# Optimization experiments

Hardware: AMD Instinct MI355X
Metric: run time of the kernel (lower is better)

Reference implementation:

```python
import jax, jax.numpy as jnp
import numpy as np

D_MODEL = 1024; D_STATE = 64; D_CONV = 4; EXPAND = 2; HEADDIM = 128; NGROUPS = 1; CHUNK = 256
D_INNER = EXPAND * D_MODEL            # 2048
NHEADS = D_INNER // HEADDIM           # 16
CONV_DIM = D_INNER + 2 * NGROUPS * D_STATE   # 2176
D_IN_PROJ = 2 * D_INNER + 2 * NGROUPS * D_STATE + NHEADS  # 4240
B = 4; G = 256; L = 2048
EPS = 1e-5


def setup_inputs() -> dict:
    key = jax.random.key(0)
    ks = jax.random.split(key, 12)
    def nrm(k, shape, s=0.02):
        return jax.random.normal(k, shape, jnp.float32) * s
    return dict(
        local_repr=jax.random.normal(ks[0], (B, L, D_MODEL), jnp.float32),
        global_repr=jax.random.normal(ks[1], (B, G, D_MODEL), jnp.float32),
        norm1_w=jnp.ones((D_MODEL,), jnp.float32), norm1_b=jnp.zeros((D_MODEL,), jnp.float32),
        norm2_w=jnp.ones((D_MODEL,), jnp.float32), norm2_b=jnp.zeros((D_MODEL,), jnp.float32),
        norm3_w=jnp.ones((D_MODEL,), jnp.float32), norm3_b=jnp.zeros((D_MODEL,), jnp.float32),
        in_proj_w=nrm(ks[2], (D_IN_PROJ, D_MODEL)),
        conv_w=nrm(ks[3], (CONV_DIM, D_CONV), 0.2),
        conv_b=jnp.zeros((CONV_DIM,), jnp.float32),
        dt_bias=jnp.log(jnp.expm1(jax.random.uniform(ks[4], (NHEADS,), jnp.float32, 1e-3, 0.1))),
        A_log=jnp.log(jax.random.uniform(ks[5], (NHEADS,), jnp.float32, 1.0, 16.0)),
        D_skip=jnp.ones((NHEADS,), jnp.float32),
        ssd_norm_w=jnp.ones((D_INNER,), jnp.float32),
        out_proj_w=nrm(ks[6], (D_MODEL, D_INNER)),
        ffn_w1=nrm(ks[7], (D_MODEL // 2, D_MODEL)),
        ffn_b1=jnp.zeros((D_MODEL // 2,), jnp.float32),
        ffn_w2=nrm(ks[8], (D_MODEL, D_MODEL // 2)),
        ffn_b2=jnp.zeros((D_MODEL,), jnp.float32),
    )


def _ln(x, w, b):
    mu = jnp.mean(x, axis=-1, keepdims=True)
    var = jnp.mean((x - mu) ** 2, axis=-1, keepdims=True)
    return (x - mu) * jax.lax.rsqrt(var + EPS) * w + b


def _segsum(a):
    # a: (..., T) -> (..., T, T) lower-triangular sums a[j+1..i]
    T = a.shape[-1]
    cs = jnp.cumsum(a, axis=-1)
    diff = cs[..., :, None] - cs[..., None, :]
    mask = jnp.tril(jnp.ones((T, T), bool))
    return jnp.where(mask, diff, -jnp.inf)


def _ssd(xdt, a_dt, Bh, Ch):
    # xdt: (b,t,h,p) = x*dt ; a_dt: (b,t,h) = dt*A ; Bh,Ch: (b,t,h,n)
    b, t, h, p = xdt.shape
    n = Bh.shape[-1]
    c = t // CHUNK
    X = xdt.reshape(b, c, CHUNK, h, p)
    Bc = Bh.reshape(b, c, CHUNK, h, n)
    Cc = Ch.reshape(b, c, CHUNK, h, n)
    Ac = a_dt.reshape(b, c, CHUNK, h).transpose(0, 3, 1, 2)  # (b,h,c,k)
    A_cum = jnp.cumsum(Ac, axis=-1)
    Lm = jnp.exp(_segsum(Ac))                                # (b,h,c,k,k)
    Y_diag = jnp.einsum('bckhn,bcshn,bhcks,bcshp->bckhp', Cc, Bc, Lm, X)
    decay_states = jnp.exp(A_cum[..., -1:] - A_cum)          # (b,h,c,k)
    states = jnp.einsum('bckhn,bhck,bckhp->bchpn', Bc, decay_states, X)
    A_last = jnp.pad(A_cum[..., -1], ((0, 0), (0, 0), (1, 0)))
    decay_chunk = jnp.exp(_segsum(A_last))                   # (b,h,c+1,c+1)
    states = jnp.concatenate([jnp.zeros_like(states[:, :1]), states], axis=1)
    new_states = jnp.einsum('bhzc,bchpn->bzhpn', decay_chunk, states)
    states_in = new_states[:, :-1]                           # (b,c,h,p,n)
    out_decay = jnp.exp(A_cum)                               # (b,h,c,k)
    Y_off = jnp.einsum('bckhn,bchpn,bhck->bckhp', Cc, states_in, out_decay)
    return (Y_diag + Y_off).reshape(b, t, h, p)


def _mamba2(x, in_proj_w, conv_w, conv_b, dt_bias, A_log, D_skip, ssd_norm_w, out_proj_w):
    b, t, _ = x.shape
    zxbcdt = x @ in_proj_w.T                                  # (b,t,D_IN_PROJ)
    z = zxbcdt[..., :D_INNER]
    xBC = zxbcdt[..., D_INNER:D_INNER + CONV_DIM]
    dt = jax.nn.softplus(zxbcdt[..., D_INNER + CONV_DIM:] + dt_bias)  # (b,t,h)
    # causal depthwise conv1d, kernel D_CONV
    xp = jnp.pad(xBC, ((0, 0), (D_CONV - 1, 0), (0, 0)))
    xBC = sum(xp[:, i:i + t, :] * conv_w[:, i] for i in range(D_CONV)) + conv_b
    xBC = jax.nn.silu(xBC)
    xs = xBC[..., :D_INNER].reshape(b, t, NHEADS, HEADDIM)
    Bm = xBC[..., D_INNER:D_INNER + NGROUPS * D_STATE].reshape(b, t, NGROUPS, D_STATE)
    Cm = xBC[..., D_INNER + NGROUPS * D_STATE:].reshape(b, t, NGROUPS, D_STATE)
    rep = NHEADS // NGROUPS
    Bh = jnp.repeat(Bm, rep, axis=2)
    Ch = jnp.repeat(Cm, rep, axis=2)
    A = -jnp.exp(A_log)                                       # (h,)
    Y = _ssd(xs * dt[..., None], dt * A, Bh, Ch)
    y = Y + D_skip[None, None, :, None] * xs
    y = y.reshape(b, t, D_INNER)
    # gated RMSNorm (norm_before_gate=False)
    y = y * jax.nn.silu(z)
    y = y * jax.lax.rsqrt(jnp.mean(y * y, axis=-1, keepdims=True) + EPS) * ssd_norm_w
    return y @ out_proj_w.T


def reference(local_repr, global_repr, norm1_w, norm1_b, norm2_w, norm2_b, norm3_w, norm3_b,
              in_proj_w, conv_w, conv_b, dt_bias, A_log, D_skip, ssd_norm_w, out_proj_w,
              ffn_w1, ffn_b1, ffn_w2, ffn_b2):
    local_n = _ln(local_repr, norm1_w, norm1_b)
    global_n = _ln(global_repr, norm2_w, norm2_b)
    x = jnp.concatenate([global_n, local_n], axis=1)          # (B, G+L, D)
    x = _mamba2(x, in_proj_w, conv_w, conv_b, dt_bias, A_log, D_skip, ssd_norm_w, out_proj_w)
    x = x[:, -local_n.shape[1]:, :] + local_n
    x = _ln(x, norm3_w, norm3_b)
    h = jax.nn.gelu(x @ ffn_w1.T + ffn_b1, approximate=False)
    return (h @ ffn_w2.T + ffn_b2) + x
```

## Files before the change

### kernel.cpp

```cpp
#include <hip/hip_runtime.h>
#include <math.h>

#define B_ 4
#define L_ 2048
#define G_ 256
#define T_ 2304
#define DM 1024
#define DINNER 2048
#define NH 16
#define HD 128
#define NSTATE 64
#define CONVD 2176
#define DPROJ 4240
#define NPROJ_PAD 4352
#define NCHUNK 9
#define CK 256
#define EPSV 1e-5f
#define CROWS 16

typedef unsigned short bf16t;
using bf16x8 = __attribute__((ext_vector_type(8))) short;
using f32x4  = __attribute__((ext_vector_type(4))) float;

__device__ __forceinline__ float bf2f(bf16t u) {
  return __uint_as_float(((unsigned int)u) << 16);
}
__device__ __forceinline__ bf16t f2bf(float f) {
  unsigned int u = __float_as_uint(f);
  u += 0x7FFFu + ((u >> 16) & 1u);
  return (bf16t)(u >> 16);
}

__device__ __forceinline__ void g2lds16(const bf16t* g, short* l) {
  __builtin_amdgcn_global_load_lds(
      (const __attribute__((address_space(1))) unsigned int*)g,
      (__attribute__((address_space(3))) unsigned int*)l, 16, 0, 0);
}

__device__ __forceinline__ int2 xcd_swz(int tiles_n) {
  int gx = gridDim.x, gy = gridDim.y;
  int id = blockIdx.y * gx + blockIdx.x;
  int cpx = (gx * gy) >> 3;
  int L = (id & 7) * cpx + (id >> 3);
  return make_int2(L % tiles_n, L / tiles_n);
}

__device__ __forceinline__ float2 block_reduce2(float a, float b) {
  __shared__ float sa[4], sb[4];
  #pragma unroll
  for (int off = 32; off > 0; off >>= 1) {
    a += __shfl_down(a, off, 64);
    b += __shfl_down(b, off, 64);
  }
  int lane = threadIdx.x & 63, wid = threadIdx.x >> 6;
  if (lane == 0) { sa[wid] = a; sb[wid] = b; }
  __syncthreads();
  return make_float2(sa[0] + sa[1] + sa[2] + sa[3], sb[0] + sb[1] + sb[2] + sb[3]);
}

__global__ __launch_bounds__(256) void ln_cvt_kernel(
    const float* __restrict__ localr, const float* __restrict__ globalr,
    const float* __restrict__ w1, const float* __restrict__ b1,
    const float* __restrict__ w2, const float* __restrict__ b2,
    bf16t* __restrict__ x, const float* __restrict__ inpw,
    bf16t* __restrict__ inpw_bf) {
  int blk = blockIdx.x;
  if (blk < B_ * T_) {
    int t = blk % T_, b = blk / T_;
    const float *src, *w, *bb;
    if (t < G_) { src = globalr + ((long)b * G_ + t) * DM;        w = w2; bb = b2; }
    else        { src = localr  + ((long)b * L_ + (t - G_)) * DM; w = w1; bb = b1; }
    int d = threadIdx.x * 4;
    float4 v = *(const float4*)&src[d];
    float s = v.x + v.y + v.z + v.w;
    float sq = v.x * v.x + v.y * v.y + v.z * v.z + v.w * v.w;
    float2 r2 = block_reduce2(s, sq);
    float mu = r2.x * (1.f / DM);
    float var = r2.y * (1.f / DM) - mu * mu;
    float rstd = rsqrtf(var + EPSV);
    float4 wv = *(const float4*)&w[d];
    float4 bv = *(const float4*)&bb[d];
    ushort4 o;
    o.x = f2bf((v.x - mu) * rstd * wv.x + bv.x);
    o.y = f2bf((v.y - mu) * rstd * wv.y + bv.y);
    o.z = f2bf((v.z - mu) * rstd * wv.z + bv.z);
    o.w = f2bf((v.w - mu) * rstd * wv.w + bv.w);
    *(ushort4*)&x[(long)blk * DM + d] = o;
  } else {
    long i = (long)(blk - B_ * T_) * 1024 + threadIdx.x * 4;
    const long nreal = (long)DPROJ * DM, ntot = (long)NPROJ_PAD * DM;
    if (i < ntot) {
      ushort4 o = {0, 0, 0, 0};
      if (i < nreal) {
        float4 v = *(const float4*)&inpw[i];
        o.x = f2bf(v.x); o.y = f2bf(v.y); o.z = f2bf(v.z); o.w = f2bf(v.w);
      }
      *(ushort4*)&inpw_bf[i] = o;
    }
  }
}

template<int EPI, bool OFFS, int K>
__global__ __launch_bounds__(512, 2) void gemm_wide(
    const bf16t* __restrict__ A, const bf16t* __restrict__ W,
    bf16t* __restrict__ Cb, bf16t* __restrict__ z, bf16t* __restrict__ xpre,
    float* __restrict__ dtr, const float* __restrict__ bias,
    const bf16t* __restrict__ res, float* __restrict__ Cf, int N) {
  __shared__ short LDS8[65536];
  int tid = threadIdx.x;
  int lane = tid & 63, w = tid >> 6;
  int wm = w >> 1, wn = w & 1;
  int l15 = lane & 15;
  int2 sz = xcd_swz(gridDim.x);
  int bn = sz.x * 128, bm = sz.y * 256;
  if (EPI == 0 && bn < DINNER && (bm % 2304) == 0) return;
  long bmA = OFFS ? ((long)(bm >> 11) * T_ + G_ + (bm & 2047)) : (long)bm;

  int csub = ((lane & 7) ^ (lane >> 3)) * 8;
  const bf16t* srcA = A + (bmA + w * 16 + (lane >> 3)) * (long)K + csub;
  const bf16t* srcW = W + (long)(bn + w * 16 + (lane >> 3)) * K + csub;
  int stageDst = w * 1024 + lane * 8;

  int off0 = l15 * 64 + (((lane >> 4) + 0) ^ (lane & 7)) * 8;
  int off1 = l15 * 64 + (((lane >> 4) + 4) ^ (lane & 7)) * 8;

  f32x4 acc[4][4] = {};
  bf16x8 af[2][2], bq[4][2];

#define STAGE2(gsrc, ldsoff) do { \
    g2lds16((gsrc), LDS8 + (ldsoff) + stageDst); \
    g2lds16((gsrc) + 8 * (long)K, LDS8 + (ldsoff) + stageDst + 512); } while (0)

  STAGE2(srcA, 0);
  STAGE2(srcA + 128 * (long)K, 8192);
  STAGE2(srcW, 49152);
  STAGE2(srcA + 64, 16384);
  STAGE2(srcA + 128 * (long)K + 64, 16384 + 8192);
  STAGE2(srcW + 64, 49152 + 8192);
  asm volatile("s_waitcnt vmcnt(6)" ::: "memory");
  __builtin_amdgcn_s_barrier();

  const int nt = K >> 6;
  for (int t = 0; t < nt; ++t) {
    int slotA = (t % 3) * 16384;
    int slotA2 = ((t + 2) % 3) * 16384;
    const short* aB = LDS8 + slotA + wm * 4096;
    const short* bB = LDS8 + 49152 + (t & 1) * 8192 + wn * 4096;

    #pragma unroll
    for (int mi = 0; mi < 2; mi++) {
      af[mi][0] = *(const bf16x8*)&aB[mi * 1024 + off0];
      af[mi][1] = *(const bf16x8*)&aB[mi * 1024 + off1];
    }
    #pragma unroll
    for (int ni = 0; ni < 2; ni++) {
      bq[ni][0] = *(const bf16x8*)&bB[ni * 1024 + off0];
      bq[ni][1] = *(const bf16x8*)&bB[ni * 1024 + off1];
    }
    if (t + 2 < nt) STAGE2(srcA + (t + 2) * 64, slotA2);
    __builtin_amdgcn_s_barrier();
    __builtin_amdgcn_s_setprio(1);
    #pragma unroll
    for (int ks = 0; ks < 2; ks++)
      #pragma unroll
      for (int mi = 0; mi < 2; mi++)
        #pragma unroll
        for (int ni = 0; ni < 2; ni++)
          acc[mi][ni] = __builtin_amdgcn_mfma_f32_16x16x32_bf16(af[mi][ks], bq[ni][ks], acc[mi][ni], 0, 0, 0);
    __builtin_amdgcn_s_setprio(0);
    __builtin_amdgcn_s_barrier();

    #pragma unroll
    for (int ni = 2; ni < 4; ni++) {
      bq[ni][0] = *(const bf16x8*)&bB[ni * 1024 + off0];
      bq[ni][1] = *(const bf16x8*)&bB[ni * 1024 + off1];
    }
    if (t + 2 < nt) STAGE2(srcA + 128 * (long)K + (t + 2) * 64, slotA2 + 8192);
    __builtin_amdgcn_s_barrier();
    __builtin_amdgcn_s_setprio(1);
    #pragma unroll
    for (int ks = 0; ks < 2; ks++)
      #pragma unroll
      for (int mi = 0; mi < 2; mi++)
        #pragma unroll
        for (int ni = 2; ni < 4; ni++)
          acc[mi][ni] = __builtin_amdgcn_mfma_f32_16x16x32_bf16(af[mi][ks], bq[ni][ks], acc[mi][ni], 0, 0, 0);
    __builtin_amdgcn_s_setprio(0);
    __builtin_amdgcn_s_barrier();

    #pragma unroll
    for (int mi = 0; mi < 2; mi++) {
      af[mi][0] = *(const bf16x8*)&aB[(mi + 2) * 1024 + off0];
      af[mi][1] = *(const bf16x8*)&aB[(mi + 2) * 1024 + off1];
    }
    if (t + 2 < nt) STAGE2(srcW + (t + 2) * 64, 49152 + (t & 1) * 8192);
    __builtin_amdgcn_s_barrier();
    __builtin_amdgcn_s_setprio(1);
    #pragma unroll
    for (int ks = 0; ks < 2; ks++)
      #pragma unroll
      for (int mi = 0; mi < 2; mi++)
        #pragma unroll
        for (int ni = 0; ni < 4; ni++)
          acc[mi + 2][ni] = __builtin_amdgcn_mfma_f32_16x16x32_bf16(af[mi][ks], bq[ni][ks], acc[mi + 2][ni], 0, 0, 0);
    __builtin_amdgcn_s_setprio(0);
    if (t + 2 < nt)      asm volatile("s_waitcnt vmcnt(6)" ::: "memory");
    else if (t + 1 < nt) asm volatile("s_waitcnt vmcnt(0)" ::: "memory");
    __builtin_amdgcn_s_barrier();
  }
#undef STAGE2

  if (EPI == 0 && bn == 4224) {
    if (wn == 0) {
      #pragma unroll
      for (int mi = 0; mi < 4; mi++)
        #pragma unroll
        for (int r = 0; r < 4; r++) {
          int row = bm + wm * 64 + mi * 16 + (lane >> 4) * 4 + r;
          dtr[(long)row * NH + l15] = acc[mi][0][r];
        }
    }
    return;
  }

  if (EPI == 2) {
    float* Cs32 = (float*)LDS8;
    #pragma unroll
    for (int pass = 0; pass < 2; pass++) {
      __syncthreads();
      if ((wm >> 1) == pass) {
        #pragma unroll
        for (int mi = 0; mi < 4; mi++)
          #pragma unroll
          for (int ni = 0; ni < 4; ni++)
            #pragma unroll
            for (int r = 0; r < 4; r++)
              Cs32[((wm & 1) * 64 + mi * 16 + (lane >> 4) * 4 + r) * 136 + wn * 64 + ni * 16 + l15] =
                  acc[mi][ni][r];
      }
      __syncthreads();
      #pragma unroll
      for (int q = 0; q < 4; q++) {
        int idx = q * 512 + tid;
        int row = idx >> 4, cg = (idx & 15) * 8;
        long grow = bm + pass * 128 + row; int gcol = bn + cg;
        float4 v0 = *(float4*)&Cs32[row * 136 + cg];
        float4 v1 = *(float4*)&Cs32[row * 136 + cg + 4];
        float4 b0 = *(const float4*)&bias[gcol];
        float4 b1 = *(const float4*)&bias[gcol + 4];
        bf16x8 rv = *(const bf16x8*)&res[grow * (long)N + gcol];
        v0.x += b0.x + bf2f((bf16t)rv[0]); v0.y += b0.y + bf2f((bf16t)rv[1]);
        v0.z += b0.z + bf2f((bf16t)rv[2]); v0.w += b0.w + bf2f((bf16t)rv[3]);
        v1.x += b1.x + bf2f((bf16t)rv[4]); v1.y += b1.y + bf2f((bf16t)rv[5]);
        v1.z += b1.z + bf2f((bf16t)rv[6]); v1.w += b1.w + bf2f((bf16t)rv[7]);
        *(float4*)&Cf[grow * (long)N + gcol] = v0;
        *(float4*)&Cf[grow * (long)N + gcol + 4] = v1;
      }
    }
    return;
  }

  bf16t* Cs = (bf16t*)LDS8;
  #pragma unroll
  for (int pass = 0; pass < 2; pass++) {
    __syncthreads();
    if ((wm >> 1) == pass) {
      #pragma unroll
      for (int mi = 0; mi < 4; mi++)
        #pragma unroll
        for (int ni = 0; ni < 4; ni++)
          #pragma unroll
          for (int r = 0; r < 4; r++)
            Cs[((wm & 1) * 64 + mi * 16 + (lane >> 4) * 4 + r) * 136 + wn * 64 + ni * 16 + l15] =
                f2bf(acc[mi][ni][r]);
    }
    __syncthreads();
    #pragma unroll
    for (int q = 0; q < 4; q++) {
      int idx = q * 512 + tid;
      int row = idx >> 4, cg = idx & 15;
      int gcol = bn + cg * 8;
      long grow = bm + pass * 128 + row;
      bf16x8 v = *(bf16x8*)&Cs[row * 136 + cg * 8];
      if (EPI == 0) {
        if (gcol < DINNER) *(bf16x8*)&z[grow * DINNER + gcol] = v;
        else               *(bf16x8*)&xpre[grow * CONVD + (gcol - DINNER)] = v;
      } else {
        *(bf16x8*)&Cb[grow * (long)N + gcol] = v;
      }
    }
  }
}

template<int EPI>
__global__ __launch_bounds__(256) void gemm_mfma(
    const bf16t* __restrict__ A, const bf16t* __restrict__ W,
    const float* __restrict__ bias, const bf16t* __restrict__ res,
    float* __restrict__ Cf, bf16t* __restrict__ Cb,
    int N, int K) {
  __shared__ __align__(16) short LDS[128 * 136];
  short* As = LDS;
  short* Ws = LDS + 128 * 32;
  int tid = threadIdx.x;
  int lane = tid & 63, w = tid >> 6;
  int wr = w >> 1, wc = w & 1;
  int2 sz = xcd_swz(gridDim.x);
  int bn = sz.x * 128, bm = sz.y * 128;

  int r1 = tid >> 2,         s1 = (((tid & 3) ^ ((r1 >> 1) & 3))) * 8;
  int r2 = (tid + 256) >> 2, s2 = (((tid & 3) ^ ((r2 >> 1) & 3))) * 8;
  const bf16t* gA1 = A + (long)(bm + r1) * K + s1;
  const bf16t* gA2 = A + (long)(bm + r2) * K + s2;
  const bf16t* gW1 = W + (long)(bn + r1) * K + s1;
  const bf16t* gW2 = W + (long)(bn + r2) * K + s2;
  short* lA1 = As + tid * 8;
  short* lA2 = As + (tid + 256) * 8;
  short* lW1 = Ws + tid * 8;
  short* lW2 = Ws + (tid + 256) * 8;

  int arow = wr * 64 + (lane & 15);
  int brow = wc * 64 + (lane & 15);
  int koff = (((lane >> 4) ^ (((lane & 15) >> 1) & 3))) * 8;

  f32x4 acc[4][4] = {};
  for (int k0 = 0; k0 < K; k0 += 32) {
    g2lds16(gA1 + k0, lA1);
    g2lds16(gA2 + k0, lA2);
    g2lds16(gW1 + k0, lW1);
    g2lds16(gW2 + k0, lW2);
    __syncthreads();
    bf16x8 af[4], bf[4];
    #pragma unroll
    for (int mi = 0; mi < 4; mi++) af[mi] = *(bf16x8*)&As[(arow + mi * 16) * 32 + koff];
    #pragma unroll
    for (int ni = 0; ni < 4; ni++) bf[ni] = *(bf16x8*)&Ws[(brow + ni * 16) * 32 + koff];
    #pragma unroll
    for (int mi = 0; mi < 4; mi++)
      #pragma unroll
      for (int ni = 0; ni < 4; ni++)
        acc[mi][ni] = __builtin_amdgcn_mfma_f32_16x16x32_bf16(af[mi], bf[ni], acc[mi][ni], 0, 0, 0);
    __syncthreads();
  }

  int rb = wr * 64 + (lane >> 4) * 4;
  int cb = wc * 64 + (lane & 15);

  __syncthreads();
  bf16t* Cs = (bf16t*)LDS;
  #pragma unroll
  for (int mi = 0; mi < 4; mi++)
    #pragma unroll
    for (int ni = 0; ni < 4; ni++)
      #pragma unroll
      for (int r = 0; r < 4; r++) {
        float v = acc[mi][ni][r];
        if (EPI == 2) {
          v += bias[bn + cb + ni * 16];
          v = 0.5f * v * (1.f + erff(v * 0.70710678118f));
        }
        Cs[(rb + mi * 16 + r) * 136 + cb + ni * 16] = f2bf(v);
      }
  __syncthreads();
  #pragma unroll
  for (int pass = 0; pass < 8; pass++) {
    int row = pass * 16 + (tid >> 4);
    int col = (tid & 15) * 8;
    bf16x8 vv = *(bf16x8*)&Cs[row * 136 + col];
    long grow = bm + row; int gcol = bn + col;
    *(bf16x8*)&Cb[grow * N + gcol] = vv;
  }
}

__global__ __launch_bounds__(256) void cumsum_kernel(
    const float* __restrict__ dtraw, const float* __restrict__ dt_bias,
    const float* __restrict__ A_log, float* __restrict__ dt,
    float* __restrict__ Acum) {
  int bid = blockIdx.x;
  int c = bid % NCHUNK; int hh = bid / NCHUNK;
  int h = hh % NH; int b = hh / NH;
  int k = threadIdx.x;
  float a = -__expf(A_log[h]);
  long t = (long)b * T_ + c * CK + k;
  float v0 = dtraw[t * NH + h] + dt_bias[h];
  float dtv = (v0 > 20.f) ? v0 : log1pf(__expf(v0));
  dt[t * NH + h] = dtv;
  float v = dtv * a;
  __shared__ float buf[2][CK];
  int cur = 0;
  buf[0][k] = v; __syncthreads();
  for (int off = 1; off < CK; off <<= 1) {
    float tv = buf[cur][k];
    if (k >= off) tv += buf[cur][k - off];
    buf[1 - cur][k] = tv; cur ^= 1; __syncthreads();
  }
  Acum[(long)bid * CK + k] = buf[cur][k];
}

__global__ __launch_bounds__(256) void conv_kernel(
    const bf16t* __restrict__ xpre, const float* __restrict__ cw,
    const float* __restrict__ cb, bf16t* __restrict__ out) {
  int gt = blockIdx.x * 256 + threadIdx.x;
  int cg = gt % 272; int rt = gt / 272;
  int c0 = cg * 8;
  long r0 = (long)rt * CROWS;
  int t0 = (int)(r0 % T_);

  float wreg[4][8];
  #pragma unroll
  for (int j = 0; j < 8; j++) {
    float4 wa = *(const float4*)&cw[(c0 + j) * 4];
    wreg[0][j] = wa.x; wreg[1][j] = wa.y; wreg[2][j] = wa.z; wreg[3][j] = wa.w;
  }
  float4 cb0 = *(const float4*)&cb[c0];
  float4 cb1 = *(const float4*)&cb[c0 + 4];
  float bias[8] = {cb0.x, cb0.y, cb0.z, cb0.w, cb1.x, cb1.y, cb1.z, cb1.w};

  bf16x8 win[4];
  #pragma unroll
  for (int i = 0; i < 3; i++) {
    if (t0 - 3 + i >= 0) win[i] = *(const bf16x8*)&xpre[(r0 - 3 + i) * CONVD + c0];
    else                 win[i] = bf16x8{0,0,0,0,0,0,0,0};
  }

  #pragma unroll
  for (int k = 0; k < CROWS; k++) {
    win[3] = *(const bf16x8*)&xpre[(r0 + k) * CONVD + c0];
    float acc[8];
    #pragma unroll
    for (int j = 0; j < 8; j++) acc[j] = bias[j];
    #pragma unroll
    for (int i = 0; i < 4; i++)
      #pragma unroll
      for (int j = 0; j < 8; j++)
        acc[j] += bf2f((bf16t)win[i][j]) * wreg[i][j];
    bf16x8 o;
    #pragma unroll
    for (int j = 0; j < 8; j++) {
      float s = acc[j] / (1.f + __expf(-acc[j]));
      o[j] = (short)f2bf(s);
    }
    *(bf16x8*)&out[(r0 + k) * CONVD + c0] = o;
    win[0] = win[1]; win[1] = win[2]; win[2] = win[3];
  }
}

__global__ __launch_bounds__(256) void chunk_states_kernel(
    const bf16t* __restrict__ xbc, const float* __restrict__ dt,
    const float* __restrict__ Acum, float* __restrict__ cs) {
  int bid = blockIdx.x;
  int h = bid & 15; int bc = bid >> 4;
  int c = bc & 7; int b = bc >> 3;
  int tid = threadIdx.x;
  int lane = tid & 63, w = tid >> 6;
  long tch = (long)b * T_ + c * CK;
  int acb = ((b * NH + h) * NCHUNK + c) * CK;
  float Alast = Acum[acb + CK - 1];

  __shared__ bf16t Xt[128][72];
  __shared__ bf16t Bt[64][72];
  __shared__ float wk[64];

  f32x4 acc[8] = {};
  for (int kb = 0; kb < 4; kb++) {
    int s0 = kb * 64;
    __syncthreads();
    if (tid < 64)
      wk[tid] = __expf(Alast - Acum[acb + s0 + tid]) * dt[(tch + s0 + tid) * NH + h];
    __syncthreads();
    for (int e = tid; e < 64 * 32; e += 256) {
      int s = e & 63, p4 = e >> 6;
      ushort4 u = *(const ushort4*)&xbc[(tch + s0 + s) * CONVD + h * HD + p4 * 4];
      float wv = wk[s];
      Xt[p4 * 4 + 0][s] = f2bf(bf2f(u.x) * wv);
      Xt[p4 * 4 + 1][s] = f2bf(bf2f(u.y) * wv);
      Xt[p4 * 4 + 2][s] = f2bf(bf2f(u.z) * wv);
      Xt[p4 * 4 + 3][s] = f2bf(bf2f(u.w) * wv);
    }
    for (int e = tid; e < 64 * 16; e += 256) {
      int s = e & 63, n4 = e >> 6;
      ushort4 u = *(const ushort4*)&xbc[(tch + s0 + s) * CONVD + DINNER + n4 * 4];
      Bt[n4 * 4 + 0][s] = u.x; Bt[n4 * 4 + 1][s] = u.y;
      Bt[n4 * 4 + 2][s] = u.z; Bt[n4 * 4 + 3][s] = u.w;
    }
    __syncthreads();
    #pragma unroll
    for (int ks = 0; ks < 2; ks++) {
      int koff = (lane >> 4) * 8 + ks * 32;
      bf16x8 bfr = *(bf16x8*)&Bt[w * 16 + (lane & 15)][koff];
      #pragma unroll
      for (int mi = 0; mi < 8; mi++) {
        bf16x8 af = *(bf16x8*)&Xt[mi * 16 + (lane & 15)][koff];
        acc[mi] = __builtin_amdgcn_mfma_f32_16x16x32_bf16(af, bfr, acc[mi], 0, 0, 0);
      }
    }
  }
  int cbid = (b * NCHUNK + c) * NH + h;
  float* out = cs + (long)cbid * HD * NSTATE;
  int n = w * 16 + (lane & 15);
  #pragma unroll
  for (int mi = 0; mi < 8; mi++) {
    #pragma unroll
    for (int r = 0; r < 4; r++) {
      int p = mi * 16 + (lane >> 4) * 4 + r;
      out[p * NSTATE + n] = acc[mi][r];
    }
  }
}

__global__ __launch_bounds__(256) void state_pass_kernel(
    float* __restrict__ cs, const float* __restrict__ Acum) {
  int bh = blockIdx.x;
  int b = bh / NH, h = bh % NH;
  int e0 = blockIdx.y * 1024 + threadIdx.x;
  for (int q = 0; q < 4; q++) {
    int e = e0 + q * 256;
    float s = 0.f;
    for (int c = 0; c < NCHUNK; c++) {
      long idx = ((long)(b * NCHUNK + c) * NH + h) * (HD * NSTATE) + e;
      if (c < NCHUNK - 1) {
        float tmp = cs[idx];
        cs[idx] = s;
        float g = __expf(Acum[((b * NH + h) * NCHUNK + c) * CK + CK - 1]);
        s = s * g + tmp;
      } else {
        cs[idx] = s;
      }
    }
  }
}

__global__ __launch_bounds__(256) void ssd_y_kernel(
    const bf16t* __restrict__ xbc, const float* __restrict__ dt,
    const float* __restrict__ Acum, const float* __restrict__ sin_,
    const float* __restrict__ Dskip, bf16t* __restrict__ Y) {
  int bid = blockIdx.x;
  int h = bid & 15; int bc = bid >> 4;
  int c = 1 + (bc & 7); int b = bc >> 3;
  int rt = blockIdx.y;
  int tid = threadIdx.x;
  int lane = tid & 63, w = tid >> 6;
  int wr = w >> 1, wc = w & 1;
  long tch = (long)b * T_ + c * CK;
  long tbase = tch + rt * 128;
  int acb = ((b * NH + h) * NCHUNK + c) * CK;

  __shared__ bf16t Cs[128][72];
  __shared__ bf16t Bs[64][72];
  __shared__ bf16t Xt[128][72];
  __shared__ bf16t Sm[128][72];
  __shared__ float Akl[128];
  __shared__ float Asl[64];
  __shared__ float dts[64];

  for (int e = tid; e < 128 * 8; e += 256) {
    int row = e >> 3, seg = (e & 7) * 8;
    *(bf16x8*)&Cs[row][seg] =
        *(const bf16x8*)&xbc[(tbase + row) * CONVD + DINNER + NSTATE + seg];
  }
  if (tid < 128) Akl[tid] = Acum[acb + rt * 128 + tid];

  f32x4 acc[4][4] = {};
  int nsb = 2 * (rt + 1);
  for (int sb = 0; sb < nsb; sb++) {
    int s0 = sb * 64;
    __syncthreads();
    if (tid < 64) {
      Asl[tid] = Acum[acb + s0 + tid];
      dts[tid] = dt[(tch + s0 + tid) * NH + h];
    }
    __syncthreads();
    for (int e = tid; e < 64 * 8; e += 256) {
      int row = e >> 3, seg = (e & 7) * 8;
      *(bf16x8*)&Bs[row][seg] =
          *(const bf16x8*)&xbc[(tch + s0 + row) * CONVD + DINNER + seg];
    }
    for (int e = tid; e < 64 * 32; e += 256) {
      int s = e & 63, p4 = e >> 6;
      ushort4 u = *(const ushort4*)&xbc[(tch + s0 + s) * CONVD + h * HD + p4 * 4];
      float dtv = dts[s];
      Xt[p4 * 4 + 0][s] = f2bf(bf2f(u.x) * dtv);
      Xt[p4 * 4 + 1][s] = f2bf(bf2f(u.y) * dtv);
      Xt[p4 * 4 + 2][s] = f2bf(bf2f(u.z) * dtv);
      Xt[p4 * 4 + 3][s] = f2bf(bf2f(u.w) * dtv);
    }
    __syncthreads();
    {
      f32x4 sacc[2][4] = {};
      int rw0 = w * 32;
      #pragma unroll
      for (int ks = 0; ks < 2; ks++) {
        int koff = (lane >> 4) * 8 + ks * 32;
        bf16x8 a0 = *(bf16x8*)&Cs[rw0 + (lane & 15)][koff];
        bf16x8 a1 = *(bf16x8*)&Cs[rw0 + 16 + (lane & 15)][koff];
        #pragma unroll
        for (int ni = 0; ni < 4; ni++) {
          bf16x8 bfr = *(bf16x8*)&Bs[ni * 16 + (lane & 15)][koff];
          sacc[0][ni] = __builtin_amdgcn_mfma_f32_16x16x32_bf16(a0, bfr, sacc[0][ni], 0, 0, 0);
          sacc[1][ni] = __builtin_amdgcn_mfma_f32_16x16x32_bf16(a1, bfr, sacc[1][ni], 0, 0, 0);
        }
      }
      #pragma unroll
      for (int mi = 0; mi < 2; mi++) {
        #pragma unroll
        for (int ni = 0; ni < 4; ni++) {
          #pragma unroll
          for (int r = 0; r < 4; r++) {
            int row = rw0 + mi * 16 + (lane >> 4) * 4 + r;
            int scol = ni * 16 + (lane & 15);
            int kglob = rt * 128 + row;
            int sglob = s0 + scol;
            float val = 0.f;
            if (sglob <= kglob) val = sacc[mi][ni][r] * __expf(Akl[row] - Asl[scol]);
            Sm[row][scol] = f2bf(val);
          }
        }
      }
    }
    __syncthreads();
    #pragma unroll
    for (int ks = 0; ks < 2; ks++) {
      int koff = (lane >> 4) * 8 + ks * 32;
      bf16x8 af[4], bfr[4];
      #pragma unroll
      for (int mi = 0; mi < 4; mi++) af[mi] = *(bf16x8*)&Sm[wr * 64 + mi * 16 + (lane & 15)][koff];
      #pragma unroll
      for (int ni = 0; ni < 4; ni++) bfr[ni] = *(bf16x8*)&Xt[wc * 64 + ni * 16 + (lane & 15)][koff];
      #pragma unroll
      for (int mi = 0; mi < 4; mi++)
        #pragma unroll
        for (int ni = 0; ni < 4; ni++)
          acc[mi][ni] = __builtin_amdgcn_mfma_f32_16x16x32_bf16(af[mi], bfr[ni], acc[mi][ni], 0, 0, 0);
    }
  }

  float ekr[16];
  #pragma unroll
  for (int mi = 0; mi < 4; mi++)
    #pragma unroll
    for (int r = 0; r < 4; r++)
      ekr[mi * 4 + r] = __expf(Akl[wr * 64 + mi * 16 + (lane >> 4) * 4 + r]);

  int cbid = (b * NCHUNK + c) * NH + h;
  const float* sinb = sin_ + (long)cbid * HD * NSTATE;
  #pragma unroll
  for (int ni = 0; ni < 4; ni++) {
    f32x4 offacc[4] = {};
    int p = wc * 64 + ni * 16 + (lane & 15);
    #pragma unroll
    for (int ks = 0; ks < 2; ks++) {
      int koff = (lane >> 4) * 8 + ks * 32;
      const float* srow = sinb + p * NSTATE + koff;
      float4 sa = *(const float4*)srow;
      float4 sbv = *(const float4*)(srow + 4);
      bf16x8 bfr;
      bfr[0] = (short)f2bf(sa.x);  bfr[1] = (short)f2bf(sa.y);
      bfr[2] = (short)f2bf(sa.z);  bfr[3] = (short)f2bf(sa.w);
      bfr[4] = (short)f2bf(sbv.x); bfr[5] = (short)f2bf(sbv.y);
      bfr[6] = (short)f2bf(sbv.z); bfr[7] = (short)f2bf(sbv.w);
      #pragma unroll
      for (int mi = 0; mi < 4; mi++) {
        bf16x8 af = *(bf16x8*)&Cs[wr * 64 + mi * 16 + (lane & 15)][koff];
        offacc[mi] = __builtin_amdgcn_mfma_f32_16x16x32_bf16(af, bfr, offacc[mi], 0, 0, 0);
      }
    }
    #pragma unroll
    for (int mi = 0; mi < 4; mi++)
      #pragma unroll
      for (int r = 0; r < 4; r++)
        acc[mi][ni][r] += ekr[mi * 4 + r] * offacc[mi][r];
  }

  float dsk = Dskip[h];
  #pragma unroll
  for (int mi = 0; mi < 4; mi++) {
    #pragma unroll
    for (int r = 0; r < 4; r++) {
      int row = wr * 64 + mi * 16 + (lane >> 4) * 4 + r;
      long t = tbase + row;
      #pragma unroll
      for (int ni = 0; ni < 4; ni++) {
        int p = wc * 64 + ni * 16 + (lane & 15);
        float xsv = bf2f(xbc[t * CONVD + h * HD + p]);
        Y[t * DINNER + h * HD + p] = f2bf(acc[mi][ni][r] + dsk * xsv);
      }
    }
  }
}

__global__ __launch_bounds__(256) void gate_rms_cvt_kernel(
    const bf16t* __restrict__ z, const float* __restrict__ nw,
    bf16t* __restrict__ Y,
    const float* __restrict__ outw, const float* __restrict__ f1w,
    const float* __restrict__ f2w, bf16t* __restrict__ o_out,
    bf16t* __restrict__ o_f1, bf16t* __restrict__ o_f2) {
  int blk = blockIdx.x;
  if (blk < B_ * L_) {
    long r = (long)(blk >> 11) * T_ + G_ + (blk & 2047);
    const bf16t* zrow = z + r * DINNER;
    bf16t* yrow = Y + r * DINNER;
    int tid = threadIdx.x;
    float v[8]; float sq = 0.f;
    #pragma unroll
    for (int i = 0; i < 4; i++) {
      int d = tid * 2 + 512 * i;
      ushort2 zu = *(const ushort2*)&zrow[d];
      ushort2 yu = *(const ushort2*)&yrow[d];
      float z0 = bf2f(zu.x), z1 = bf2f(zu.y);
      float y0 = bf2f(yu.x) * (z0 / (1.f + __expf(-z0)));
      float y1 = bf2f(yu.y) * (z1 / (1.f + __expf(-z1)));
      v[2 * i] = y0; v[2 * i + 1] = y1;
      sq += y0 * y0 + y1 * y1;
    }
    float2 r2 = block_reduce2(sq, 0.f);
    float rms = rsqrtf(r2.x * (1.f / DINNER) + EPSV);
    #pragma unroll
    for (int i = 0; i < 4; i++) {
      int d = tid * 2 + 512 * i;
      ushort2 o;
      o.x = f2bf(v[2 * i] * rms * nw[d]);
      o.y = f2bf(v[2 * i + 1] * rms * nw[d + 1]);
      *(ushort2*)&yrow[d] = o;
    }
  } else {
    long i = (long)(blk - B_ * L_) * 1024 + threadIdx.x * 4;
    const long n1 = (long)DM * DINNER;
    const long n2 = (long)(DM / 2) * DM;
    const float* src; bf16t* dst; long off;
    if (i < n1) { src = outw; dst = o_out; off = i; }
    else if (i < n1 + n2) { src = f1w; dst = o_f1; off = i - n1; }
    else { src = f2w; dst = o_f2; off = i - n1 - n2; }
    float4 v = *(const float4*)&src[off];
    ushort4 o;
    o.x = f2bf(v.x); o.y = f2bf(v.y); o.z = f2bf(v.z); o.w = f2bf(v.w);
    *(ushort4*)&dst[off] = o;
  }
}

__global__ __launch_bounds__(256) void res_ln3_kernel(
    const bf16t* __restrict__ mfull, const bf16t* __restrict__ x,
    const float* __restrict__ w3, const float* __restrict__ b3,
    bf16t* __restrict__ x2) {
  int rl = blockIdx.x;
  int tl = rl & 2047, b = rl >> 11;
  long rt = (long)b * T_ + G_ + tl;
  const bf16t* m = mfull + (long)rl * DM;
  const bf16t* xr = x + rt * DM;
  int tid = threadIdx.x;
  float v[4]; float s = 0.f, sq = 0.f;
  #pragma unroll
  for (int i = 0; i < 2; i++) {
    int d = tid * 2 + 512 * i;
    ushort2 mu2 = *(const ushort2*)&m[d];
    ushort2 xu2 = *(const ushort2*)&xr[d];
    float a0 = bf2f(mu2.x) + bf2f(xu2.x);
    float a1 = bf2f(mu2.y) + bf2f(xu2.y);
    v[2 * i] = a0; v[2 * i + 1] = a1;
    s += a0 + a1; sq += a0 * a0 + a1 * a1;
  }
  float2 r2 = block_reduce2(s, sq);
  float mu = r2.x * (1.f / DM);
  float var = r2.y * (1.f / DM) - mu * mu;
  float rstd = rsqrtf(var + EPSV);
  bf16t* dst = x2 + (long)rl * DM;
  #pragma unroll
  for (int i = 0; i < 2; i++) {
    int d = tid * 2 + 512 * i;
    ushort2 o;
    o.x = f2bf((v[2 * i] - mu) * rstd * w3[d] + b3[d]);
    o.y = f2bf((v[2 * i + 1] - mu) * rstd * w3[d + 1] + b3[d + 1]);
    *(ushort2*)&dst[d] = o;
  }
}

extern "C" void kernel_launch(void* const* d_in, const int* in_sizes, int n_in,
                              void* d_out, int out_size, void* d_ws, size_t ws_size,
                              hipStream_t stream) {
  const float* localr = (const float*)d_in[0];
  const float* globalr= (const float*)d_in[1];
  const float* n1w = (const float*)d_in[2];
  const float* n1b = (const float*)d_in[3];
  const float* n2w = (const float*)d_in[4];
  const float* n2b = (const float*)d_in[5];
  const float* n3w = (const float*)d_in[6];
  const float* n3b = (const float*)d_in[7];
  const float* inpw= (const float*)d_in[8];
  const float* convw=(const float*)d_in[9];
  const float* convb=(const float*)d_in[10];
  const float* dtb = (const float*)d_in[11];
  const float* alog= (const float*)d_in[12];
  const float* dskp= (const float*)d_in[13];
  const float* ssdw= (const float*)d_in[14];
  const float* outw= (const float*)d_in[15];
  const float* f1w = (const float*)d_in[16];
  const float* f1b = (const float*)d_in[17];
  const float* f2w = (const float*)d_in[18];
  const float* f2b = (const float*)d_in[19];

  char* ws = (char*)d_ws;
  bf16t* x     = (bf16t*)(ws + 0);
  bf16t* z     = (bf16t*)(ws + 18874368);
  bf16t* mfull = (bf16t*)(ws + 18874368);
  bf16t* xpre  = (bf16t*)(ws + 56623104);
  bf16t* Yb    = (bf16t*)(ws + 56623104);
  float* dtraw = (float*)(ws + 96731136);
  float* dt    = (float*)(ws + 97320960);
  float* Acum  = (float*)(ws + 97910784);
  bf16t* xbc   = (bf16t*)(ws + 98500608);
  bf16t* x2bf  = (bf16t*)(ws + 98500608);
  bf16t* hbuf  = (bf16t*)(ws + 115277824);
  bf16t* outw_bf = (bf16t*)(ws + 123666432);
  bf16t* f1w_bf  = (bf16t*)(ws + 127860736);
  bf16t* f2w_bf  = (bf16t*)(ws + 128909312);
  float* cs    = (float*)(ws + 138608640);
  bf16t* inpw_bf = (bf16t*)(ws + 138608640);

  ln_cvt_kernel<<<B_ * T_ + 4352, 256, 0, stream>>>(
      localr, globalr, n1w, n1b, n2w, n2b, x, inpw, inpw_bf);

  gemm_wide<0, false, 1024><<<dim3(NPROJ_PAD / 128, (B_ * T_) / 256), 512, 0, stream>>>(
      x, inpw_bf, nullptr, z, xpre, dtraw, nullptr, nullptr, nullptr, NPROJ_PAD);

  cumsum_kernel<<<B_ * NH * NCHUNK, 256, 0, stream>>>(dtraw, dtb, alog, dt, Acum);

  conv_kernel<<<(B_ * T_ / CROWS) * 272 / 256, 256, 0, stream>>>(xpre, convw, convb, xbc);

  chunk_states_kernel<<<B_ * (NCHUNK - 1) * NH, 256, 0, stream>>>(xbc, dt, Acum, cs);

  state_pass_kernel<<<dim3(B_ * NH, 8), 256, 0, stream>>>(cs, Acum);

  ssd_y_kernel<<<dim3(B_ * (NCHUNK - 1) * NH, 2), 256, 0, stream>>>(
      xbc, dt, Acum, cs, dskp, Yb);

  gate_rms_cvt_kernel<<<B_ * L_ + 3072, 256, 0, stream>>>(
      z, ssdw, Yb, outw, f1w, f2w, outw_bf, f1w_bf, f2w_bf);

  gemm_wide<1, true, 2048><<<dim3(DM / 128, (B_ * L_) / 256), 512, 0, stream>>>(
      Yb, outw_bf, mfull, nullptr, nullptr, nullptr, nullptr, nullptr, nullptr, DM);

  res_ln3_kernel<<<B_ * L_, 256, 0, stream>>>(mfull, x, n3w, n3b, x2bf);

  gemm_mfma<2><<<dim3((DM / 2) / 128, (B_ * L_) / 128), 256, 0, stream>>>(
      x2bf, f1w_bf, f1b, nullptr, nullptr, hbuf, DM / 2, DM);

  gemm_wide<2, false, 512><<<dim3(DM / 128, (B_ * L_) / 256), 512, 0, stream>>>(
      hbuf, f2w_bf, nullptr, nullptr, nullptr, nullptr, f2b, x2bf, (float*)d_out, DM);
}
```

Before: 472.5 us.

## Merge conv and cumsum launches, vectorize LDS transposes and row kernels

Merges the conv and dt-cumsum kernels into a single launch that branches on block index, removing one launch. In the chunk-states and ssd_y loaders, each thread now reads four consecutive time rows and writes packed ushort4 values into the transposed LDS tiles, replacing scalar 16-bit LDS stores. The ssd_y epilogue stages accumulators through shared memory so that Y and the D-skip x input move as coalesced 16-byte vectors instead of scattered scalar accesses. The gated RMSNorm and the final LayerNorm row kernels switch to wider per-thread vector loads and stores. In exchange there are extra barriers in the epilogue and slightly more global loads in flight per thread.

```diff
diff --git a/kernel.cpp b/kernel.cpp
--- a/kernel.cpp
+++ b/kernel.cpp
@@ -17,6 +17,7 @@
 #define CK 256
 #define EPSV 1e-5f
 #define CROWS 16
+#define CONVBLKS 612
 
 typedef unsigned short bf16t;
 using bf16x8 = __attribute__((ext_vector_type(8))) short;
@@ -371,76 +372,76 @@
   }
 }
 
-__global__ __launch_bounds__(256) void cumsum_kernel(
+__global__ __launch_bounds__(256) void conv_cumsum_kernel(
+    const bf16t* __restrict__ xpre, const float* __restrict__ cw,
+    const float* __restrict__ cb, bf16t* __restrict__ out,
     const float* __restrict__ dtraw, const float* __restrict__ dt_bias,
     const float* __restrict__ A_log, float* __restrict__ dt,
     float* __restrict__ Acum) {
-  int bid = blockIdx.x;
-  int c = bid % NCHUNK; int hh = bid / NCHUNK;
-  int h = hh % NH; int b = hh / NH;
-  int k = threadIdx.x;
-  float a = -__expf(A_log[h]);
-  long t = (long)b * T_ + c * CK + k;
-  float v0 = dtraw[t * NH + h] + dt_bias[h];
-  float dtv = (v0 > 20.f) ? v0 : log1pf(__expf(v0));
-  dt[t * NH + h] = dtv;
-  float v = dtv * a;
-  __shared__ float buf[2][CK];
-  int cur = 0;
-  buf[0][k] = v; __syncthreads();
-  for (int off = 1; off < CK; off <<= 1) {
-    float tv = buf[cur][k];
-    if (k >= off) tv += buf[cur][k - off];
-    buf[1 - cur][k] = tv; cur ^= 1; __syncthreads();
-  }
-  Acum[(long)bid * CK + k] = buf[cur][k];
-}
-
-__global__ __launch_bounds__(256) void conv_kernel(
-    const bf16t* __restrict__ xpre, const float* __restrict__ cw,
-    const float* __restrict__ cb, bf16t* __restrict__ out) {
-  int gt = blockIdx.x * 256 + threadIdx.x;
-  int cg = gt % 272; int rt = gt / 272;
-  int c0 = cg * 8;
-  long r0 = (long)rt * CROWS;
-  int t0 = (int)(r0 % T_);
-
-  float wreg[4][8];
-  #pragma unroll
-  for (int j = 0; j < 8; j++) {
-    float4 wa = *(const float4*)&cw[(c0 + j) * 4];
-    wreg[0][j] = wa.x; wreg[1][j] = wa.y; wreg[2][j] = wa.z; wreg[3][j] = wa.w;
-  }
-  float4 cb0 = *(const float4*)&cb[c0];
-  float4 cb1 = *(const float4*)&cb[c0 + 4];
-  float bias[8] = {cb0.x, cb0.y, cb0.z, cb0.w, cb1.x, cb1.y, cb1.z, cb1.w};
-
-  bf16x8 win[4];
-  #pragma unroll
-  for (int i = 0; i < 3; i++) {
-    if (t0 - 3 + i >= 0) win[i] = *(const bf16x8*)&xpre[(r0 - 3 + i) * CONVD + c0];
-    else                 win[i] = bf16x8{0,0,0,0,0,0,0,0};
-  }
-
-  #pragma unroll
-  for (int k = 0; k < CROWS; k++) {
-    win[3] = *(const bf16x8*)&xpre[(r0 + k) * CONVD + c0];
-    float acc[8];
-    #pragma unroll
-    for (int j = 0; j < 8; j++) acc[j] = bias[j];
-    #pragma unroll
-    for (int i = 0; i < 4; i++)
-      #pragma unroll
-      for (int j = 0; j < 8; j++)
-        acc[j] += bf2f((bf16t)win[i][j]) * wreg[i][j];
-    bf16x8 o;
+  if (blockIdx.x < CONVBLKS) {
+    int gt = blockIdx.x * 256 + threadIdx.x;
+    int cg = gt % 272; int rt = gt / 272;
+    int c0 = cg * 8;
+    long r0 = (long)rt * CROWS;
+    int t0 = (int)(r0 % T_);
+
+    float wreg[4][8];
     #pragma unroll
     for (int j = 0; j < 8; j++) {
-      float s = acc[j] / (1.f + __expf(-acc[j]));
-      o[j] = (short)f2bf(s);
-    }
-    *(bf16x8*)&out[(r0 + k) * CONVD + c0] = o;
-    win[0] = win[1]; win[1] = win[2]; win[2] = win[3];
+      float4 wa = *(const float4*)&cw[(c0 + j) * 4];
+      wreg[0][j] = wa.x; wreg[1][j] = wa.y; wreg[2][j] = wa.z; wreg[3][j] = wa.w;
+    }
+    float4 cb0 = *(const float4*)&cb[c0];
+    float4 cb1 = *(const float4*)&cb[c0 + 4];
+    float bias[8] = {cb0.x, cb0.y, cb0.z, cb0.w, cb1.x, cb1.y, cb1.z, cb1.w};
+
+    bf16x8 win[4];
+    #pragma unroll
+    for (int i = 0; i < 3; i++) {
+      if (t0 - 3 + i >= 0) win[i] = *(const bf16x8*)&xpre[(r0 - 3 + i) * CONVD + c0];
+      else                 win[i] = bf16x8{0,0,0,0,0,0,0,0};
+    }
+
+    #pragma unroll
+    for (int k = 0; k < CROWS; k++) {
+      win[3] = *(const bf16x8*)&xpre[(r0 + k) * CONVD + c0];
+      float acc[8];
+      #pragma unroll
+      for (int j = 0; j < 8; j++) acc[j] = bias[j];
+      #pragma unroll
+      for (int i = 0; i < 4; i++)
+        #pragma unroll
+        for (int j = 0; j < 8; j++)
+          acc[j] += bf2f((bf16t)win[i][j]) * wreg[i][j];
+      bf16x8 o;
+      #pragma unroll
+      for (int j = 0; j < 8; j++) {
+        float s = acc[j] / (1.f + __expf(-acc[j]));
+        o[j] = (short)f2bf(s);
+      }
+      *(bf16x8*)&out[(r0 + k) * CONVD + c0] = o;
+      win[0] = win[1]; win[1] = win[2]; win[2] = win[3];
+    }
+  } else {
+    int bid = blockIdx.x - CONVBLKS;
+    int c = bid % NCHUNK; int hh = bid / NCHUNK;
+    int h = hh % NH; int b = hh / NH;
+    int k = threadIdx.x;
+    float a = -__expf(A_log[h]);
+    long t = (long)b * T_ + c * CK + k;
+    float v0 = dtraw[t * NH + h] + dt_bias[h];
+    float dtv = (v0 > 20.f) ? v0 : log1pf(__expf(v0));
+    dt[t * NH + h] = dtv;
+    float v = dtv * a;
+    __shared__ float buf[2][CK];
+    int cur = 0;
+    buf[0][k] = v; __syncthreads();
+    for (int off = 1; off < CK; off <<= 1) {
+      float tv = buf[cur][k];
+      if (k >= off) tv += buf[cur][k - off];
+      buf[1 - cur][k] = tv; cur ^= 1; __syncthreads();
+    }
+    Acum[(long)bid * CK + k] = buf[cur][k];
   }
 }
 
@@ -467,20 +468,44 @@
     if (tid < 64)
       wk[tid] = __expf(Alast - Acum[acb + s0 + tid]) * dt[(tch + s0 + tid) * NH + h];
     __syncthreads();
-    for (int e = tid; e < 64 * 32; e += 256) {
-      int s = e & 63, p4 = e >> 6;
-      ushort4 u = *(const ushort4*)&xbc[(tch + s0 + s) * CONVD + h * HD + p4 * 4];
-      float wv = wk[s];
-      Xt[p4 * 4 + 0][s] = f2bf(bf2f(u.x) * wv);
-      Xt[p4 * 4 + 1][s] = f2bf(bf2f(u.y) * wv);
-      Xt[p4 * 4 + 2][s] = f2bf(bf2f(u.z) * wv);
-      Xt[p4 * 4 + 3][s] = f2bf(bf2f(u.w) * wv);
-    }
-    for (int e = tid; e < 64 * 16; e += 256) {
-      int s = e & 63, n4 = e >> 6;
-      ushort4 u = *(const ushort4*)&xbc[(tch + s0 + s) * CONVD + DINNER + n4 * 4];
-      Bt[n4 * 4 + 0][s] = u.x; Bt[n4 * 4 + 1][s] = u.y;
-      Bt[n4 * 4 + 2][s] = u.z; Bt[n4 * 4 + 3][s] = u.w;
+    for (int e = tid; e < 16 * 32; e += 256) {
+      int s4 = (e & 15) * 4, p4 = e >> 4;
+      const bf16t* base = &xbc[(tch + s0 + s4) * CONVD + h * HD + p4 * 4];
+      ushort4 u0 = *(const ushort4*)(base);
+      ushort4 u1 = *(const ushort4*)(base + CONVD);
+      ushort4 u2 = *(const ushort4*)(base + 2 * CONVD);
+      ushort4 u3 = *(const ushort4*)(base + 3 * CONVD);
+      float w0 = wk[s4], w1 = wk[s4 + 1], w2 = wk[s4 + 2], w3 = wk[s4 + 3];
+      ushort4 pk;
+      pk.x = f2bf(bf2f(u0.x) * w0); pk.y = f2bf(bf2f(u1.x) * w1);
+      pk.z = f2bf(bf2f(u2.x) * w2); pk.w = f2bf(bf2f(u3.x) * w3);
+      *(ushort4*)&Xt[p4 * 4 + 0][s4] = pk;
+      pk.x = f2bf(bf2f(u0.y) * w0); pk.y = f2bf(bf2f(u1.y) * w1);
+      pk.z = f2bf(bf2f(u2.y) * w2); pk.w = f2bf(bf2f(u3.y) * w3);
+      *(ushort4*)&Xt[p4 * 4 + 1][s4] = pk;
+      pk.x = f2bf(bf2f(u0.z) * w0); pk.y = f2bf(bf2f(u1.z) * w1);
+      pk.z = f2bf(bf2f(u2.z) * w2); pk.w = f2bf(bf2f(u3.z) * w3);
+      *(ushort4*)&Xt[p4 * 4 + 2][s4] = pk;
+      pk.x = f2bf(bf2f(u0.w) * w0); pk.y = f2bf(bf2f(u1.w) * w1);
+      pk.z = f2bf(bf2f(u2.w) * w2); pk.w = f2bf(bf2f(u3.w) * w3);
+      *(ushort4*)&Xt[p4 * 4 + 3][s4] = pk;
+    }
+    for (int e = tid; e < 16 * 16; e += 256) {
+      int s4 = (e & 15) * 4, n4 = e >> 4;
+      const bf16t* base = &xbc[(tch + s0 + s4) * CONVD + DINNER + n4 * 4];
+      ushort4 u0 = *(const ushort4*)(base);
+      ushort4 u1 = *(const ushort4*)(base + CONVD);
+      ushort4 u2 = *(const ushort4*)(base + 2 * CONVD);
+      ushort4 u3 = *(const ushort4*)(base + 3 * CONVD);
+      ushort4 pk;
+      pk.x = u0.x; pk.y = u1.x; pk.z = u2.x; pk.w = u3.x;
+      *(ushort4*)&Bt[n4 * 4 + 0][s4] = pk;
+      pk.x = u0.y; pk.y = u1.y; pk.z = u2.y; pk.w = u3.y;
+      *(ushort4*)&Bt[n4 * 4 + 1][s4] = pk;
+      pk.x = u0.z; pk.y = u1.z; pk.z = u2.z; pk.w = u3.z;
+      *(ushort4*)&Bt[n4 * 4 + 2][s4] = pk;
+      pk.x = u0.w; pk.y = u1.w; pk.z = u2.w; pk.w = u3.w;
+      *(ushort4*)&Bt[n4 * 4 + 3][s4] = pk;
     }
     __syncthreads();
     #pragma unroll
@@ -546,8 +571,9 @@
 
   __shared__ bf16t Cs[128][72];
   __shared__ bf16t Bs[64][72];
-  __shared__ bf16t Xt[128][72];
-  __shared__ bf16t Sm[128][72];
+  __shared__ __align__(16) bf16t XtSm[2][128][72];
+  bf16t (*Xt)[72] = XtSm[0];
+  bf16t (*Sm)[72] = XtSm[1];
   __shared__ float Akl[128];
   __shared__ float Asl[64];
   __shared__ float dts[64];
@@ -574,14 +600,27 @@
       *(bf16x8*)&Bs[row][seg] =
           *(const bf16x8*)&xbc[(tch + s0 + row) * CONVD + DINNER + seg];
     }
-    for (int e = tid; e < 64 * 32; e += 256) {
-      int s = e & 63, p4 = e >> 6;
-      ushort4 u = *(const ushort4*)&xbc[(tch + s0 + s) * CONVD + h * HD + p4 * 4];
-      float dtv = dts[s];
-      Xt[p4 * 4 + 0][s] = f2bf(bf2f(u.x) * dtv);
-      Xt[p4 * 4 + 1][s] = f2bf(bf2f(u.y) * dtv);
-      Xt[p4 * 4 + 2][s] = f2bf(bf2f(u.z) * dtv);
-      Xt[p4 * 4 + 3][s] = f2bf(bf2f(u.w) * dtv);
+    for (int e = tid; e < 16 * 32; e += 256) {
+      int s4 = (e & 15) * 4, p4 = e >> 4;
+      const bf16t* base = &xbc[(tch + s0 + s4) * CONVD + h * HD + p4 * 4];
+      ushort4 u0 = *(const ushort4*)(base);
+      ushort4 u1 = *(const ushort4*)(base + CONVD);
+      ushort4 u2 = *(const ushort4*)(base + 2 * CONVD);
+      ushort4 u3 = *(const ushort4*)(base + 3 * CONVD);
+      float d0 = dts[s4], d1 = dts[s4 + 1], d2 = dts[s4 + 2], d3 = dts[s4 + 3];
+      ushort4 pk;
+      pk.x = f2bf(bf2f(u0.x) * d0); pk.y = f2bf(bf2f(u1.x) * d1);
+      pk.z = f2bf(bf2f(u2.x) * d2); pk.w = f2bf(bf2f(u3.x) * d3);
+      *(ushort4*)&Xt[p4 * 4 + 0][s4] = pk;
+      pk.x = f2bf(bf2f(u0.y) * d0); pk.y = f2bf(bf2f(u1.y) * d1);
+      pk.z = f2bf(bf2f(u2.y) * d2); pk.w = f2bf(bf2f(u3.y) * d3);
+      *(ushort4*)&Xt[p4 * 4 + 1][s4] = pk;
+      pk.x = f2bf(bf2f(u0.z) * d0); pk.y = f2bf(bf2f(u1.z) * d1);
+      pk.z = f2bf(bf2f(u2.z) * d2); pk.w = f2bf(bf2f(u3.z) * d3);
+      *(ushort4*)&Xt[p4 * 4 + 2][s4] = pk;
+      pk.x = f2bf(bf2f(u0.w) * d0); pk.y = f2bf(bf2f(u1.w) * d1);
+      pk.z = f2bf(bf2f(u2.w) * d2); pk.w = f2bf(bf2f(u3.w) * d3);
+      *(ushort4*)&Xt[p4 * 4 + 3][s4] = pk;
     }
     __syncthreads();
     {
@@ -671,18 +710,32 @@
   }
 
   float dsk = Dskip[h];
+  float* Sf = (float*)&XtSm[0][0][0];
   #pragma unroll
-  for (int mi = 0; mi < 4; mi++) {
-    #pragma unroll
-    for (int r = 0; r < 4; r++) {
-      int row = wr * 64 + mi * 16 + (lane >> 4) * 4 + r;
-      long t = tbase + row;
-      #pragma unroll
-      for (int ni = 0; ni < 4; ni++) {
-        int p = wc * 64 + ni * 16 + (lane & 15);
-        float xsv = bf2f(xbc[t * CONVD + h * HD + p]);
-        Y[t * DINNER + h * HD + p] = f2bf(acc[mi][ni][r] + dsk * xsv);
-      }
+  for (int rh = 0; rh < 2; rh++) {
+    __syncthreads();
+    if (wr == rh) {
+      #pragma unroll
+      for (int mi = 0; mi < 4; mi++)
+        #pragma unroll
+        for (int ni = 0; ni < 4; ni++)
+          #pragma unroll
+          for (int r = 0; r < 4; r++)
+            Sf[(mi * 16 + (lane >> 4) * 4 + r) * 130 + wc * 64 + ni * 16 + (lane & 15)] =
+                acc[mi][ni][r];
+    }
+    __syncthreads();
+    #pragma unroll
+    for (int g = 0; g < 4; g++) {
+      int idx = g * 256 + tid;
+      int row = idx >> 4, cg = (idx & 15) * 8;
+      long t = tbase + rh * 64 + row;
+      bf16x8 xv = *(const bf16x8*)&xbc[t * CONVD + h * HD + cg];
+      bf16x8 o;
+      #pragma unroll
+      for (int j = 0; j < 8; j++)
+        o[j] = (short)f2bf(Sf[row * 130 + cg + j] + dsk * bf2f((bf16t)xv[j]));
+      *(bf16x8*)&Y[t * DINNER + h * HD + cg] = o;
     }
   }
 }
@@ -699,28 +752,25 @@
     const bf16t* zrow = z + r * DINNER;
     bf16t* yrow = Y + r * DINNER;
     int tid = threadIdx.x;
+    int d = tid * 8;
+    bf16x8 zu = *(const bf16x8*)&zrow[d];
+    bf16x8 yu = *(const bf16x8*)&yrow[d];
     float v[8]; float sq = 0.f;
     #pragma unroll
-    for (int i = 0; i < 4; i++) {
-      int d = tid * 2 + 512 * i;
-      ushort2 zu = *(const ushort2*)&zrow[d];
-      ushort2 yu = *(const ushort2*)&yrow[d];
-      float z0 = bf2f(zu.x), z1 = bf2f(zu.y);
-      float y0 = bf2f(yu.x) * (z0 / (1.f + __expf(-z0)));
-      float y1 = bf2f(yu.y) * (z1 / (1.f + __expf(-z1)));
-      v[2 * i] = y0; v[2 * i + 1] = y1;
-      sq += y0 * y0 + y1 * y1;
+    for (int j = 0; j < 8; j++) {
+      float z0 = bf2f((bf16t)zu[j]);
+      float y0 = bf2f((bf16t)yu[j]) * (z0 / (1.f + __expf(-z0)));
+      v[j] = y0; sq += y0 * y0;
     }
     float2 r2 = block_reduce2(sq, 0.f);
     float rms = rsqrtf(r2.x * (1.f / DINNER) + EPSV);
-    #pragma unroll
-    for (int i = 0; i < 4; i++) {
-      int d = tid * 2 + 512 * i;
-      ushort2 o;
-      o.x = f2bf(v[2 * i] * rms * nw[d]);
-      o.y = f2bf(v[2 * i + 1] * rms * nw[d + 1]);
-      *(ushort2*)&yrow[d] = o;
-    }
+    float4 nw0 = *(const float4*)&nw[d];
+    float4 nw1 = *(const float4*)&nw[d + 4];
+    float nn[8] = {nw0.x, nw0.y, nw0.z, nw0.w, nw1.x, nw1.y, nw1.z, nw1.w};
+    bf16x8 o;
+    #pragma unroll
+    for (int j = 0; j < 8; j++) o[j] = (short)f2bf(v[j] * rms * nn[j]);
+    *(bf16x8*)&yrow[d] = o;
   } else {
     long i = (long)(blk - B_ * L_) * 1024 + threadIdx.x * 4;
     const long n1 = (long)DM * DINNER;
@@ -746,30 +796,28 @@
   const bf16t* m = mfull + (long)rl * DM;
   const bf16t* xr = x + rt * DM;
   int tid = threadIdx.x;
-  float v[4]; float s = 0.f, sq = 0.f;
-  #pragma unroll
-  for (int i = 0; i < 2; i++) {
-    int d = tid * 2 + 512 * i;
-    ushort2 mu2 = *(const ushort2*)&m[d];
-    ushort2 xu2 = *(const ushort2*)&xr[d];
-    float a0 = bf2f(mu2.x) + bf2f(xu2.x);
-    float a1 = bf2f(mu2.y) + bf2f(xu2.y);
-    v[2 * i] = a0; v[2 * i + 1] = a1;
-    s += a0 + a1; sq += a0 * a0 + a1 * a1;
-  }
+  int d = tid * 4;
+  ushort4 mu4 = *(const ushort4*)&m[d];
+  ushort4 xu4 = *(const ushort4*)&xr[d];
+  float v[4];
+  v[0] = bf2f(mu4.x) + bf2f(xu4.x);
+  v[1] = bf2f(mu4.y) + bf2f(xu4.y);
+  v[2] = bf2f(mu4.z) + bf2f(xu4.z);
+  v[3] = bf2f(mu4.w) + bf2f(xu4.w);
+  float s = v[0] + v[1] + v[2] + v[3];
+  float sq = v[0]*v[0] + v[1]*v[1] + v[2]*v[2] + v[3]*v[3];
   float2 r2 = block_reduce2(s, sq);
   float mu = r2.x * (1.f / DM);
   float var = r2.y * (1.f / DM) - mu * mu;
   float rstd = rsqrtf(var + EPSV);
-  bf16t* dst = x2 + (long)rl * DM;
-  #pragma unroll
-  for (int i = 0; i < 2; i++) {
-    int d = tid * 2 + 512 * i;
-    ushort2 o;
-    o.x = f2bf((v[2 * i] - mu) * rstd * w3[d] + b3[d]);
-    o.y = f2bf((v[2 * i + 1] - mu) * rstd * w3[d + 1] + b3[d + 1]);
-    *(ushort2*)&dst[d] = o;
-  }
+  float4 w4 = *(const float4*)&w3[d];
+  float4 b4 = *(const float4*)&b3[d];
+  ushort4 o;
+  o.x = f2bf((v[0] - mu) * rstd * w4.x + b4.x);
+  o.y = f2bf((v[1] - mu) * rstd * w4.y + b4.y);
+  o.z = f2bf((v[2] - mu) * rstd * w4.z + b4.z);
+  o.w = f2bf((v[3] - mu) * rstd * w4.w + b4.w);
+  *(ushort4*)&x2[(long)rl * DM + d] = o;
 }
 
 extern "C" void kernel_launch(void* const* d_in, const int* in_sizes, int n_in,
@@ -820,9 +868,8 @@
   gemm_wide<0, false, 1024><<<dim3(NPROJ_PAD / 128, (B_ * T_) / 256), 512, 0, stream>>>(
       x, inpw_bf, nullptr, z, xpre, dtraw, nullptr, nullptr, nullptr, NPROJ_PAD);
 
-  cumsum_kernel<<<B_ * NH * NCHUNK, 256, 0, stream>>>(dtraw, dtb, alog, dt, Acum);
-
-  conv_kernel<<<(B_ * T_ / CROWS) * 272 / 256, 256, 0, stream>>>(xpre, convw, convb, xbc);
+  conv_cumsum_kernel<<<CONVBLKS + B_ * NH * NCHUNK, 256, 0, stream>>>(
+      xpre, convw, convb, xbc, dtraw, dtb, alog, dt, Acum);
 
   chunk_states_kernel<<<B_ * (NCHUNK - 1) * NH, 256, 0, stream>>>(xbc, dt, Acum, cs);
 
```

After: 450.0 us. -4.8%, faster.
